# Kernel tuning notes

Hardware: AMD Instinct MI355X
Metric: run time of the kernel (lower is better)

Reference implementation:

```python
import jax, jax.numpy as jnp
import numpy as np

D_MODEL = 1024
N_EXPERTS = 8
HIDDEN = 2048
TOP_K = 2


def setup_inputs() -> dict:
    key = jax.random.key(0)
    ks = jax.random.split(key, 5)
    scale_in = 1.0 / np.sqrt(D_MODEL)
    scale_h = 1.0 / np.sqrt(HIDDEN)
    return {
        "x": jax.random.normal(ks[0], (2, 2048, D_MODEL), dtype=jnp.float32),
        "w_router": jax.random.normal(ks[1], (D_MODEL, N_EXPERTS), dtype=jnp.float32) * scale_in,
        "w1": jax.random.normal(ks[2], (N_EXPERTS, D_MODEL, HIDDEN), dtype=jnp.float32) * scale_in,
        "w3": jax.random.normal(ks[3], (N_EXPERTS, D_MODEL, HIDDEN), dtype=jnp.float32) * scale_in,
        "w2": jax.random.normal(ks[4], (N_EXPERTS, HIDDEN, D_MODEL), dtype=jnp.float32) * scale_h,
    }


def reference(x, w_router, w1, w3, w2):
    orig_shape = x.shape
    xt = x.reshape(-1, orig_shape[-1])            # [T, D]
    T = xt.shape[0]

    # Router: linear -> softmax -> top-k (weights = top-k softmax scores)
    logits = xt @ w_router                         # [T, E]
    scores = jax.nn.softmax(logits, axis=-1)       # [T, E]
    top_w, top_idx = jax.lax.top_k(scores, TOP_K)  # [T, K]

    # Dense routing-weight matrix (reference form of dispatch/combine)
    dense_w = jnp.zeros((T, N_EXPERTS), dtype=scores.dtype)
    dense_w = dense_w.at[jnp.arange(T)[:, None], top_idx].set(top_w)  # [T, E]

    # Per-expert SwiGLU MLP over all tokens (dense reference of grouped GEMM)
    h1 = jnp.einsum('td,edh->teh', xt, w1)         # [T, E, H]
    h3 = jnp.einsum('td,edh->teh', xt, w3)
    h = jax.nn.silu(h1) * h3                       # [T, E, H]
    y = jnp.einsum('teh,ehd->ted', h, w2)          # [T, E, D]

    # Combine with routing weights
    out = jnp.einsum('te,ted->td', dense_w, y)     # [T, D]
    return out.reshape(orig_shape)
```

## Files before the change

### kernel.cpp

```cpp
#include <hip/hip_runtime.h>
#include <stdint.h>

#define D_MODEL 1024
#define N_EXP   8
#define HIDDEN  2048
#define TOPK    2

#define BK    64
#define BM    128
#define BN1   64
#define BN2   128
#define NT1   (D_MODEL / BK)
#define NT2   (HIDDEN / BK)
#define MT_MAX 72
#define G1_GRID (MT_MAX * (HIDDEN / BN1))
#define G2_GRID (MT_MAX * (D_MODEL / BN2))

typedef short bf16x8 __attribute__((ext_vector_type(8)));
typedef float f32x4 __attribute__((ext_vector_type(4)));

__device__ __forceinline__ unsigned short f2bf(float f) {
    union { float f; unsigned u; } v; v.f = f;
    unsigned r = v.u + 0x7fffu + ((v.u >> 16) & 1u);
    return (unsigned short)(r >> 16);
}

__device__ __forceinline__ float bf2f(unsigned short u) {
    union { unsigned u; float f; } v; v.u = (unsigned)u << 16; return v.f;
}

__device__ __forceinline__ void gload_lds16(const void* g, void* l) {
    __builtin_amdgcn_global_load_lds(
        (const __attribute__((address_space(1))) void*)g,
        (__attribute__((address_space(3))) void*)l, 16, 0, 0);
}

__global__ __launch_bounds__(256) void k_router_cvt(
    const float* __restrict__ x, const float* __restrict__ wr,
    unsigned short* __restrict__ xb,
    int* __restrict__ tok_e, float* __restrict__ tok_w,
    int* __restrict__ counts, int T)
{
    int t = blockIdx.x * 4 + (threadIdx.x >> 6);
    int lane = threadIdx.x & 63;
    if (t >= T) return;
    const float4* xr = (const float4*)(x + (size_t)t * D_MODEL);
    float acc[N_EXP];
#pragma unroll
    for (int e = 0; e < N_EXP; ++e) acc[e] = 0.f;
#pragma unroll
    for (int j = 0; j < 4; ++j) {
        int c = j * 64 + lane;
        float4 v = xr[c];
        ushort4 pk;
        pk.x = f2bf(v.x); pk.y = f2bf(v.y); pk.z = f2bf(v.z); pk.w = f2bf(v.w);
        *(ushort4*)(xb + (size_t)t * D_MODEL + c * 4) = pk;
        const float4* w4 = (const float4*)(wr + (size_t)c * 4 * N_EXP);
#pragma unroll
        for (int k = 0; k < 4; ++k) {
            float xv = (k == 0) ? v.x : (k == 1) ? v.y : (k == 2) ? v.z : v.w;
            float4 wa = w4[k * 2], wb = w4[k * 2 + 1];
            acc[0] += xv * wa.x; acc[1] += xv * wa.y; acc[2] += xv * wa.z; acc[3] += xv * wa.w;
            acc[4] += xv * wb.x; acc[5] += xv * wb.y; acc[6] += xv * wb.z; acc[7] += xv * wb.w;
        }
    }
#pragma unroll
    for (int off = 32; off > 0; off >>= 1) {
#pragma unroll
        for (int e = 0; e < N_EXP; ++e) acc[e] += __shfl_down(acc[e], off, 64);
    }
    if (lane == 0) {
        float mx = acc[0];
#pragma unroll
        for (int e = 1; e < N_EXP; ++e) mx = fmaxf(mx, acc[e]);
        float p[N_EXP], den = 0.f;
#pragma unroll
        for (int e = 0; e < N_EXP; ++e) { p[e] = __expf(acc[e] - mx); den += p[e]; }
        float inv = 1.f / den;
        int e0 = 0; float v0 = acc[0];
#pragma unroll
        for (int e = 1; e < N_EXP; ++e) if (acc[e] > v0) { v0 = acc[e]; e0 = e; }
        int e1 = -1; float v1 = -1e30f;
#pragma unroll
        for (int e = 0; e < N_EXP; ++e) if (e != e0 && acc[e] > v1) { v1 = acc[e]; e1 = e; }
        tok_e[2 * t] = e0;     tok_w[2 * t] = p[e0] * inv;
        tok_e[2 * t + 1] = e1; tok_w[2 * t + 1] = p[e1] * inv;
        atomicAdd(&counts[e0], 1);
        atomicAdd(&counts[e1], 1);
    }
}

__global__ __launch_bounds__(256) void k_cvt3(
    const float* __restrict__ w1, const float* __restrict__ w3, const float* __restrict__ w2,
    unsigned short* __restrict__ w1t, unsigned short* __restrict__ w3t, unsigned short* __restrict__ w2t)
{
    __shared__ unsigned short t[64][68];
    const int z = blockIdx.y;
    const int mat = z >> 3, e = z & 7;
    const float* in; unsigned short* out; int Rr, Cc;
    if (mat == 0)      { in = w1; out = w1t; Rr = D_MODEL; Cc = HIDDEN; }
    else if (mat == 1) { in = w3; out = w3t; Rr = D_MODEL; Cc = HIDDEN; }
    else               { in = w2; out = w2t; Rr = HIDDEN; Cc = D_MODEL; }
    const size_t eb = (size_t)e * Rr * Cc;
    const int tpc = Cc >> 6;
    const int bx = blockIdx.x;
    const int c0 = (bx % tpc) * 64, r0 = (bx / tpc) * 64;
    const int tid = threadIdx.x;
#pragma unroll
    for (int p = 0; p < 4; ++p) {
        int li = p * 256 + tid;
        int r = li >> 4, q = li & 15;
        float4 v = *(const float4*)(in + eb + (size_t)(r0 + r) * Cc + c0 + q * 4);
        t[q * 4 + 0][r] = f2bf(v.x);
        t[q * 4 + 1][r] = f2bf(v.y);
        t[q * 4 + 2][r] = f2bf(v.z);
        t[q * 4 + 3][r] = f2bf(v.w);
    }
    __syncthreads();
#pragma unroll
    for (int p = 0; p < 2; ++p) {
        int li = p * 256 + tid;
        int c = li >> 3, j = li & 7;
        bf16x8 v = *(const bf16x8*)(&t[c][j * 8]);
        *(bf16x8*)(&out[eb + (size_t)(c0 + c) * Rr + r0 + j * 8]) = v;
    }
}

__global__ void k_scan_scatter(const int* __restrict__ counts,
                               const int* __restrict__ tok_e, const float* __restrict__ tok_w,
                               int* __restrict__ offs,
                               int* __restrict__ row_token, float* __restrict__ row_weight,
                               int* __restrict__ tok_pos, int T) {
    __shared__ int scurs[N_EXP];
    if (threadIdx.x == 0) {
        int s = 0;
        for (int e = 0; e < N_EXP; ++e) {
            offs[e] = s; scurs[e] = s;
            s += ((counts[e] + BM - 1) / BM) * BM;
        }
        offs[N_EXP] = s;
    }
    __syncthreads();
    for (int i = threadIdx.x; i < 2 * T; i += blockDim.x) {
        int e = tok_e[i];
        int pos = atomicAdd(&scurs[e], 1);
        row_token[pos] = i >> 1;
        row_weight[pos] = tok_w[i];
        tok_pos[i] = pos;
    }
}

__global__ __launch_bounds__(256) void k_gemm1(
    const unsigned short* __restrict__ xb,
    const unsigned short* __restrict__ w1t,
    const unsigned short* __restrict__ w3t,
    const int* __restrict__ row_token,
    const float* __restrict__ row_weight,
    const int* __restrict__ offs,
    unsigned short* __restrict__ h)
{
    __shared__ unsigned short A[BM * BK];
    __shared__ unsigned short B1[BN1 * BK];
    __shared__ unsigned short B3[BN1 * BK];

    const int b = blockIdx.x;
    const int bs = (b & 7) * (G1_GRID / 8) + (b >> 3);
    int e = 0, mt = 0, nt = 0, found = 0, at = 0;
#pragma unroll
    for (int ee = 0; ee < N_EXP; ++ee) {
        int me = (offs[ee + 1] - offs[ee]) >> 7;
        int te = me * (HIDDEN / BN1);
        if (!found && bs < at + te) {
            int loc = bs - at;
            nt = loc / me;
            mt = loc - nt * me;
            e = ee; found = 1;
        }
        at += te;
    }
    if (!found) return;
    const int m0 = offs[e] + mt * BM;
    const int n0 = nt * BN1;

    const int tid = threadIdx.x;
    const int lane = tid & 63, wid = tid >> 6;
    const int wm = wid >> 1, wn = wid & 1;

    const unsigned short* asrc[4];
    unsigned aoff[4];
#pragma unroll
    for (int q = 0; q < 4; ++q) {
        int c = q * 256 + tid;
        int m = c >> 3, kc = c & 7;
        int kcs = kc ^ (m & 7);
        int tok = row_token[m0 + m];
        asrc[q] = xb + (size_t)tok * D_MODEL + kcs * 8;
        aoff[q] = (unsigned)c * 8u;
    }
    const unsigned short* b1src[2];
    const unsigned short* b3src[2];
    unsigned boff[2];
#pragma unroll
    for (int q = 0; q < 2; ++q) {
        int c = q * 256 + tid;
        int n = c >> 3, kc = c & 7;
        int kcs = kc ^ (n & 7);
        b1src[q] = w1t + ((size_t)e * HIDDEN + n0 + n) * D_MODEL + kcs * 8;
        b3src[q] = w3t + ((size_t)e * HIDDEN + n0 + n) * D_MODEL + kcs * 8;
        boff[q] = (unsigned)c * 8u;
    }

    f32x4 acc1[4][2], acc3[4][2];
    const f32x4 zf = {0.f, 0.f, 0.f, 0.f};
#pragma unroll
    for (int mi = 0; mi < 4; ++mi)
#pragma unroll
        for (int ni = 0; ni < 2; ++ni) { acc1[mi][ni] = zf; acc3[mi][ni] = zf; }

    for (int kt = 0; kt < NT1; ++kt) {
        const int ko = kt * BK;
#pragma unroll
        for (int q = 0; q < 4; ++q) gload_lds16(asrc[q] + ko, &A[aoff[q]]);
#pragma unroll
        for (int q = 0; q < 2; ++q) {
            gload_lds16(b1src[q] + ko, &B1[boff[q]]);
            gload_lds16(b3src[q] + ko, &B3[boff[q]]);
        }
        __syncthreads();
#pragma unroll
        for (int kf = 0; kf < 2; ++kf) {
            bf16x8 a[4], b1f[2], b3f[2];
            int ke = kf * 32 + (lane >> 4) * 8;
#pragma unroll
            for (int mi = 0; mi < 4; ++mi) {
                int m = wm * 64 + mi * 16 + (lane & 15);
                a[mi] = *(const bf16x8*)(&A[m * BK + (ke ^ ((m & 7) * 8))]);
            }
#pragma unroll
            for (int ni = 0; ni < 2; ++ni) {
                int n = wn * 32 + ni * 16 + (lane & 15);
                int eo = n * BK + (ke ^ ((n & 7) * 8));
                b1f[ni] = *(const bf16x8*)(&B1[eo]);
                b3f[ni] = *(const bf16x8*)(&B3[eo]);
            }
#pragma unroll
            for (int mi = 0; mi < 4; ++mi)
#pragma unroll
                for (int ni = 0; ni < 2; ++ni) {
                    acc1[mi][ni] = __builtin_amdgcn_mfma_f32_16x16x32_bf16(a[mi], b1f[ni], acc1[mi][ni], 0, 0, 0);
                    acc3[mi][ni] = __builtin_amdgcn_mfma_f32_16x16x32_bf16(a[mi], b3f[ni], acc3[mi][ni], 0, 0, 0);
                }
        }
        __syncthreads();
    }

#pragma unroll
    for (int mi = 0; mi < 4; ++mi) {
#pragma unroll
        for (int r = 0; r < 4; ++r) {
            int m = wm * 64 + mi * 16 + (lane >> 4) * 4 + r;
            float wgt = row_weight[m0 + m];
            size_t rowbase = (size_t)(m0 + m) * HIDDEN + n0;
#pragma unroll
            for (int ni = 0; ni < 2; ++ni) {
                float v1 = acc1[mi][ni][r], v3 = acc3[mi][ni][r];
                float sv = v1 / (1.f + __expf(-v1));
                int n = wn * 32 + ni * 16 + (lane & 15);
                h[rowbase + n] = f2bf(sv * v3 * wgt);
            }
        }
    }
}

__global__ __launch_bounds__(256) void k_gemm2(
    const unsigned short* __restrict__ h,
    const unsigned short* __restrict__ w2t,
    const int* __restrict__ offs,
    unsigned short* __restrict__ y)
{
    __shared__ unsigned short A[BM * BK];
    __shared__ unsigned short B[BN2 * BK];

    const int b = blockIdx.x;
    const int bs = (b & 7) * (G2_GRID / 8) + (b >> 3);
    int e = 0, mt = 0, nt = 0, found = 0, at = 0;
#pragma unroll
    for (int ee = 0; ee < N_EXP; ++ee) {
        int me = (offs[ee + 1] - offs[ee]) >> 7;
        int te = me * (D_MODEL / BN2);
        if (!found && bs < at + te) {
            int loc = bs - at;
            nt = loc / me;
            mt = loc - nt * me;
            e = ee; found = 1;
        }
        at += te;
    }
    if (!found) return;
    const int m0 = offs[e] + mt * BM;
    const int n0 = nt * BN2;

    const int tid = threadIdx.x;
    const int lane = tid & 63, wid = tid >> 6;
    const int wm = wid >> 1, wn = wid & 1;

    const unsigned short* asrc[4];
    unsigned aoff[4];
#pragma unroll
    for (int q = 0; q < 4; ++q) {
        int c = q * 256 + tid;
        int m = c >> 3, kc = c & 7;
        int kcs = kc ^ (m & 7);
        asrc[q] = h + (size_t)(m0 + m) * HIDDEN + kcs * 8;
        aoff[q] = (unsigned)c * 8u;
    }
    const unsigned short* bsrc[4];
    unsigned boff[4];
#pragma unroll
    for (int q = 0; q < 4; ++q) {
        int c = q * 256 + tid;
        int n = c >> 3, kc = c & 7;
        int kcs = kc ^ (n & 7);
        bsrc[q] = w2t + ((size_t)e * D_MODEL + n0 + n) * HIDDEN + kcs * 8;
        boff[q] = (unsigned)c * 8u;
    }

    f32x4 acc[4][4];
    const f32x4 zf = {0.f, 0.f, 0.f, 0.f};
#pragma unroll
    for (int mi = 0; mi < 4; ++mi)
#pragma unroll
        for (int ni = 0; ni < 4; ++ni) acc[mi][ni] = zf;

    for (int kt = 0; kt < NT2; ++kt) {
        const int ko = kt * BK;
#pragma unroll
        for (int q = 0; q < 4; ++q) gload_lds16(asrc[q] + ko, &A[aoff[q]]);
#pragma unroll
        for (int q = 0; q < 4; ++q) gload_lds16(bsrc[q] + ko, &B[boff[q]]);
        __syncthreads();
#pragma unroll
        for (int kf = 0; kf < 2; ++kf) {
            bf16x8 a[4], bfr[4];
            int ke = kf * 32 + (lane >> 4) * 8;
#pragma unroll
            for (int mi = 0; mi < 4; ++mi) {
                int m = wm * 64 + mi * 16 + (lane & 15);
                a[mi] = *(const bf16x8*)(&A[m * BK + (ke ^ ((m & 7) * 8))]);
            }
#pragma unroll
            for (int ni = 0; ni < 4; ++ni) {
                int n = wn * 64 + ni * 16 + (lane & 15);
                bfr[ni] = *(const bf16x8*)(&B[n * BK + (ke ^ ((n & 7) * 8))]);
            }
#pragma unroll
            for (int mi = 0; mi < 4; ++mi)
#pragma unroll
                for (int ni = 0; ni < 4; ++ni)
                    acc[mi][ni] = __builtin_amdgcn_mfma_f32_16x16x32_bf16(a[mi], bfr[ni], acc[mi][ni], 0, 0, 0);
        }
        __syncthreads();
    }

#pragma unroll
    for (int mi = 0; mi < 4; ++mi) {
#pragma unroll
        for (int r = 0; r < 4; ++r) {
            int m = wm * 64 + mi * 16 + (lane >> 4) * 4 + r;
            size_t rowbase = (size_t)(m0 + m) * D_MODEL + n0;
#pragma unroll
            for (int ni = 0; ni < 4; ++ni) {
                int n = wn * 64 + ni * 16 + (lane & 15);
                y[rowbase + n] = f2bf(acc[mi][ni][r]);
            }
        }
    }
}

__global__ void k_combine(const unsigned short* __restrict__ y,
                          const int* __restrict__ tok_pos,
                          float* __restrict__ out, int n8) {
    int i = blockIdx.x * blockDim.x + threadIdx.x;
    if (i >= n8) return;
    int t = i >> 7;
    int c = (i & 127) * 8;
    int p0 = tok_pos[2 * t];
    int p1 = tok_pos[2 * t + 1];
    bf16x8 v0 = *(const bf16x8*)(y + (size_t)p0 * D_MODEL + c);
    bf16x8 v1 = *(const bf16x8*)(y + (size_t)p1 * D_MODEL + c);
    float* op = out + (size_t)t * D_MODEL + c;
    float4 o0, o1;
    o0.x = bf2f((unsigned short)v0[0]) + bf2f((unsigned short)v1[0]);
    o0.y = bf2f((unsigned short)v0[1]) + bf2f((unsigned short)v1[1]);
    o0.z = bf2f((unsigned short)v0[2]) + bf2f((unsigned short)v1[2]);
    o0.w = bf2f((unsigned short)v0[3]) + bf2f((unsigned short)v1[3]);
    o1.x = bf2f((unsigned short)v0[4]) + bf2f((unsigned short)v1[4]);
    o1.y = bf2f((unsigned short)v0[5]) + bf2f((unsigned short)v1[5]);
    o1.z = bf2f((unsigned short)v0[6]) + bf2f((unsigned short)v1[6]);
    o1.w = bf2f((unsigned short)v0[7]) + bf2f((unsigned short)v1[7]);
    *(float4*)op = o0;
    *(float4*)(op + 4) = o1;
}

extern "C" void kernel_launch(void* const* d_in, const int* in_sizes, int n_in,
                              void* d_out, int out_size, void* d_ws, size_t ws_size,
                              hipStream_t stream) {
    const float* x  = (const float*)d_in[0];
    const float* wr = (const float*)d_in[1];
    const float* w1 = (const float*)d_in[2];
    const float* w3 = (const float*)d_in[3];
    const float* w2 = (const float*)d_in[4];
    float* out = (float*)d_out;

    const int T = in_sizes[0] / D_MODEL;
    const int Rp = T * TOPK + N_EXP * BM;

    char* ws = (char*)d_ws;
    size_t o = 0;
    unsigned short* xb  = (unsigned short*)(ws + o); o += (size_t)T * D_MODEL * 2;
    unsigned short* h   = (unsigned short*)(ws + o); o += (size_t)Rp * HIDDEN * 2;
    unsigned short* w1t = (unsigned short*)(ws + o); o += (size_t)N_EXP * D_MODEL * HIDDEN * 2;
    unsigned short* w3t = (unsigned short*)(ws + o); o += (size_t)N_EXP * D_MODEL * HIDDEN * 2;
    unsigned short* w2t = (unsigned short*)(ws + o); o += (size_t)N_EXP * HIDDEN * D_MODEL * 2;
    int*   row_token  = (int*)(ws + o);   o += (size_t)Rp * 4;
    float* row_weight = (float*)(ws + o); o += (size_t)Rp * 4;
    int*   tok_e      = (int*)(ws + o);   o += (size_t)2 * T * 4;
    float* tok_w      = (float*)(ws + o); o += (size_t)2 * T * 4;
    int*   tok_pos    = (int*)(ws + o);   o += (size_t)2 * T * 4;
    int*   counts     = (int*)(ws + o);   o += 16 * 4;
    int*   offs       = (int*)(ws + o);   o += 16 * 4;

    unsigned short* y = w1t;

    hipMemsetAsync(counts, 0, 16 * 4, stream);
    hipMemsetAsync(row_token, 0, (size_t)Rp * 4, stream);
    hipMemsetAsync(row_weight, 0, (size_t)Rp * 4, stream);

    k_router_cvt<<<(T + 3) / 4, 256, 0, stream>>>(x, wr, xb, tok_e, tok_w, counts, T);

    dim3 gc(512, 24);
    k_cvt3<<<gc, 256, 0, stream>>>(w1, w3, w2, w1t, w3t, w2t);

    k_scan_scatter<<<1, 1024, 0, stream>>>(counts, tok_e, tok_w, offs,
                                           row_token, row_weight, tok_pos, T);

    k_gemm1<<<G1_GRID, 256, 0, stream>>>(xb, w1t, w3t, row_token, row_weight, offs, h);
    k_gemm2<<<G2_GRID, 256, 0, stream>>>(h, w2t, offs, y);

    int n8 = T * D_MODEL / 8;
    k_combine<<<(n8 + 255) / 256, 256, 0, stream>>>(y, tok_pos, out, n8);
}
```

Measured before the change: 339.4 us.

## Interleave w1/w3 weights, enlarge GEMM tiles to 256 and double-buffer LDS

The weight-conversion kernel now writes w1 and w3 interleaved in 16-row groups into one combined matrix, so gemm1 loads a single B tile that covers both gate and up projections. Both GEMMs move to 512-thread blocks with larger tiles (256x256 in gemm1, 128x256 in gemm2), double-buffered LDS prefetch and s_setprio around the MFMA loops. Expert padding grows to 256 rows. The aim is more data reuse per tile and overlap of global-to-LDS loads with compute, at the cost of more padded rows, higher register and LDS pressure, and fewer blocks.

```diff
diff --git a/kernel.cpp b/kernel.cpp
--- a/kernel.cpp
+++ b/kernel.cpp
@@ -7,14 +7,14 @@
 #define TOPK    2
 
 #define BK    64
-#define BM    128
-#define BN1   64
-#define BN2   128
+#define PADM  256
 #define NT1   (D_MODEL / BK)
 #define NT2   (HIDDEN / BK)
-#define MT_MAX 72
-#define G1_GRID (MT_MAX * (HIDDEN / BN1))
-#define G2_GRID (MT_MAX * (D_MODEL / BN2))
+#define MT1_MAX 40
+#define NB1   (2 * HIDDEN / 256)
+#define G1_GRID (MT1_MAX * NB1)
+#define MT2_MAX 80
+#define G2_GRID (MT2_MAX * (D_MODEL / 256))
 
 typedef short bf16x8 __attribute__((ext_vector_type(8)));
 typedef float f32x4 __attribute__((ext_vector_type(4)));
@@ -92,16 +92,16 @@
 
 __global__ __launch_bounds__(256) void k_cvt3(
     const float* __restrict__ w1, const float* __restrict__ w3, const float* __restrict__ w2,
-    unsigned short* __restrict__ w1t, unsigned short* __restrict__ w3t, unsigned short* __restrict__ w2t)
+    unsigned short* __restrict__ w13t, unsigned short* __restrict__ w2t)
 {
     __shared__ unsigned short t[64][68];
     const int z = blockIdx.y;
     const int mat = z >> 3, e = z & 7;
-    const float* in; unsigned short* out; int Rr, Cc;
-    if (mat == 0)      { in = w1; out = w1t; Rr = D_MODEL; Cc = HIDDEN; }
-    else if (mat == 1) { in = w3; out = w3t; Rr = D_MODEL; Cc = HIDDEN; }
-    else               { in = w2; out = w2t; Rr = HIDDEN; Cc = D_MODEL; }
-    const size_t eb = (size_t)e * Rr * Cc;
+    const float* in; int Rr, Cc;
+    if (mat == 0)      { in = w1; Rr = D_MODEL; Cc = HIDDEN; }
+    else if (mat == 1) { in = w3; Rr = D_MODEL; Cc = HIDDEN; }
+    else               { in = w2; Rr = HIDDEN; Cc = D_MODEL; }
+    const size_t eb_in = (size_t)e * Rr * Cc;
     const int tpc = Cc >> 6;
     const int bx = blockIdx.x;
     const int c0 = (bx % tpc) * 64, r0 = (bx / tpc) * 64;
@@ -110,19 +110,34 @@
     for (int p = 0; p < 4; ++p) {
         int li = p * 256 + tid;
         int r = li >> 4, q = li & 15;
-        float4 v = *(const float4*)(in + eb + (size_t)(r0 + r) * Cc + c0 + q * 4);
+        float4 v = *(const float4*)(in + eb_in + (size_t)(r0 + r) * Cc + c0 + q * 4);
         t[q * 4 + 0][r] = f2bf(v.x);
         t[q * 4 + 1][r] = f2bf(v.y);
         t[q * 4 + 2][r] = f2bf(v.z);
         t[q * 4 + 3][r] = f2bf(v.w);
     }
     __syncthreads();
-#pragma unroll
-    for (int p = 0; p < 2; ++p) {
-        int li = p * 256 + tid;
-        int c = li >> 3, j = li & 7;
-        bf16x8 v = *(const bf16x8*)(&t[c][j * 8]);
-        *(bf16x8*)(&out[eb + (size_t)(c0 + c) * Rr + r0 + j * 8]) = v;
+    if (mat < 2) {
+        const size_t eb = (size_t)e * (2 * HIDDEN) * D_MODEL;
+        const int moff = mat ? 16 : 0;
+#pragma unroll
+        for (int p = 0; p < 2; ++p) {
+            int li = p * 256 + tid;
+            int c = li >> 3, j = li & 7;
+            int C = c0 + c;
+            int r13 = ((C >> 4) << 5) + moff + (C & 15);
+            bf16x8 v = *(const bf16x8*)(&t[c][j * 8]);
+            *(bf16x8*)(&w13t[eb + (size_t)r13 * D_MODEL + r0 + j * 8]) = v;
+        }
+    } else {
+        const size_t eb = (size_t)e * D_MODEL * HIDDEN;
+#pragma unroll
+        for (int p = 0; p < 2; ++p) {
+            int li = p * 256 + tid;
+            int c = li >> 3, j = li & 7;
+            bf16x8 v = *(const bf16x8*)(&t[c][j * 8]);
+            *(bf16x8*)(&w2t[eb + (size_t)(c0 + c) * HIDDEN + r0 + j * 8]) = v;
+        }
     }
 }
 
@@ -136,7 +151,7 @@
         int s = 0;
         for (int e = 0; e < N_EXP; ++e) {
             offs[e] = s; scurs[e] = s;
-            s += ((counts[e] + BM - 1) / BM) * BM;
+            s += ((counts[e] + PADM - 1) / PADM) * PADM;
         }
         offs[N_EXP] = s;
     }
@@ -150,26 +165,24 @@
     }
 }
 
-__global__ __launch_bounds__(256) void k_gemm1(
+__global__ __launch_bounds__(512, 2) void k_gemm1(
     const unsigned short* __restrict__ xb,
-    const unsigned short* __restrict__ w1t,
-    const unsigned short* __restrict__ w3t,
+    const unsigned short* __restrict__ w13t,
     const int* __restrict__ row_token,
     const float* __restrict__ row_weight,
     const int* __restrict__ offs,
     unsigned short* __restrict__ h)
 {
-    __shared__ unsigned short A[BM * BK];
-    __shared__ unsigned short B1[BN1 * BK];
-    __shared__ unsigned short B3[BN1 * BK];
+    __shared__ unsigned short A[2][256 * BK];
+    __shared__ unsigned short B[2][256 * BK];
 
     const int b = blockIdx.x;
     const int bs = (b & 7) * (G1_GRID / 8) + (b >> 3);
     int e = 0, mt = 0, nt = 0, found = 0, at = 0;
 #pragma unroll
     for (int ee = 0; ee < N_EXP; ++ee) {
-        int me = (offs[ee + 1] - offs[ee]) >> 7;
-        int te = me * (HIDDEN / BN1);
+        int me = (offs[ee + 1] - offs[ee]) >> 8;
+        int te = me * NB1;
         if (!found && bs < at + te) {
             int loc = bs - at;
             nt = loc / me;
@@ -179,107 +192,111 @@
         at += te;
     }
     if (!found) return;
-    const int m0 = offs[e] + mt * BM;
-    const int n0 = nt * BN1;
+    const int m0 = offs[e] + mt * 256;
+    const int n0b = nt * 256;
 
     const int tid = threadIdx.x;
     const int lane = tid & 63, wid = tid >> 6;
-    const int wm = wid >> 1, wn = wid & 1;
+    const int wm = wid >> 2, wn = wid & 3;
 
     const unsigned short* asrc[4];
     unsigned aoff[4];
 #pragma unroll
     for (int q = 0; q < 4; ++q) {
-        int c = q * 256 + tid;
+        int c = q * 512 + tid;
         int m = c >> 3, kc = c & 7;
         int kcs = kc ^ (m & 7);
         int tok = row_token[m0 + m];
         asrc[q] = xb + (size_t)tok * D_MODEL + kcs * 8;
         aoff[q] = (unsigned)c * 8u;
     }
-    const unsigned short* b1src[2];
-    const unsigned short* b3src[2];
-    unsigned boff[2];
-#pragma unroll
-    for (int q = 0; q < 2; ++q) {
-        int c = q * 256 + tid;
+    const unsigned short* bsrc[4];
+    unsigned boff[4];
+#pragma unroll
+    for (int q = 0; q < 4; ++q) {
+        int c = q * 512 + tid;
         int n = c >> 3, kc = c & 7;
         int kcs = kc ^ (n & 7);
-        b1src[q] = w1t + ((size_t)e * HIDDEN + n0 + n) * D_MODEL + kcs * 8;
-        b3src[q] = w3t + ((size_t)e * HIDDEN + n0 + n) * D_MODEL + kcs * 8;
+        bsrc[q] = w13t + ((size_t)e * (2 * HIDDEN) + n0b + n) * D_MODEL + kcs * 8;
         boff[q] = (unsigned)c * 8u;
     }
 
-    f32x4 acc1[4][2], acc3[4][2];
+    f32x4 acc[8][4];
     const f32x4 zf = {0.f, 0.f, 0.f, 0.f};
 #pragma unroll
-    for (int mi = 0; mi < 4; ++mi)
-#pragma unroll
-        for (int ni = 0; ni < 2; ++ni) { acc1[mi][ni] = zf; acc3[mi][ni] = zf; }
+    for (int mi = 0; mi < 8; ++mi)
+#pragma unroll
+        for (int ni = 0; ni < 4; ++ni) acc[mi][ni] = zf;
+
+#pragma unroll
+    for (int q = 0; q < 4; ++q) {
+        gload_lds16(asrc[q], &A[0][aoff[q]]);
+        gload_lds16(bsrc[q], &B[0][boff[q]]);
+    }
+    __syncthreads();
 
     for (int kt = 0; kt < NT1; ++kt) {
-        const int ko = kt * BK;
-#pragma unroll
-        for (int q = 0; q < 4; ++q) gload_lds16(asrc[q] + ko, &A[aoff[q]]);
-#pragma unroll
-        for (int q = 0; q < 2; ++q) {
-            gload_lds16(b1src[q] + ko, &B1[boff[q]]);
-            gload_lds16(b3src[q] + ko, &B3[boff[q]]);
+        const int cur = kt & 1;
+        if (kt + 1 < NT1) {
+            const int ko = (kt + 1) * BK;
+#pragma unroll
+            for (int q = 0; q < 4; ++q) {
+                gload_lds16(asrc[q] + ko, &A[cur ^ 1][aoff[q]]);
+                gload_lds16(bsrc[q] + ko, &B[cur ^ 1][boff[q]]);
+            }
+        }
+#pragma unroll
+        for (int kf = 0; kf < 2; ++kf) {
+            bf16x8 a[8], bf[4];
+            int ke = kf * 32 + (lane >> 4) * 8;
+#pragma unroll
+            for (int mi = 0; mi < 8; ++mi) {
+                int m = wm * 128 + mi * 16 + (lane & 15);
+                a[mi] = *(const bf16x8*)(&A[cur][m * BK + (ke ^ ((m & 7) * 8))]);
+            }
+#pragma unroll
+            for (int ni = 0; ni < 4; ++ni) {
+                int n = wn * 64 + ni * 16 + (lane & 15);
+                bf[ni] = *(const bf16x8*)(&B[cur][n * BK + (ke ^ ((n & 7) * 8))]);
+            }
+            __builtin_amdgcn_s_setprio(1);
+#pragma unroll
+            for (int mi = 0; mi < 8; ++mi)
+#pragma unroll
+                for (int ni = 0; ni < 4; ++ni)
+                    acc[mi][ni] = __builtin_amdgcn_mfma_f32_16x16x32_bf16(a[mi], bf[ni], acc[mi][ni], 0, 0, 0);
+            __builtin_amdgcn_s_setprio(0);
         }
         __syncthreads();
-#pragma unroll
-        for (int kf = 0; kf < 2; ++kf) {
-            bf16x8 a[4], b1f[2], b3f[2];
-            int ke = kf * 32 + (lane >> 4) * 8;
-#pragma unroll
-            for (int mi = 0; mi < 4; ++mi) {
-                int m = wm * 64 + mi * 16 + (lane & 15);
-                a[mi] = *(const bf16x8*)(&A[m * BK + (ke ^ ((m & 7) * 8))]);
-            }
-#pragma unroll
-            for (int ni = 0; ni < 2; ++ni) {
-                int n = wn * 32 + ni * 16 + (lane & 15);
-                int eo = n * BK + (ke ^ ((n & 7) * 8));
-                b1f[ni] = *(const bf16x8*)(&B1[eo]);
-                b3f[ni] = *(const bf16x8*)(&B3[eo]);
-            }
-#pragma unroll
-            for (int mi = 0; mi < 4; ++mi)
-#pragma unroll
-                for (int ni = 0; ni < 2; ++ni) {
-                    acc1[mi][ni] = __builtin_amdgcn_mfma_f32_16x16x32_bf16(a[mi], b1f[ni], acc1[mi][ni], 0, 0, 0);
-                    acc3[mi][ni] = __builtin_amdgcn_mfma_f32_16x16x32_bf16(a[mi], b3f[ni], acc3[mi][ni], 0, 0, 0);
-                }
-        }
-        __syncthreads();
-    }
-
-#pragma unroll
-    for (int mi = 0; mi < 4; ++mi) {
+    }
+
+    const int g0 = (n0b + wn * 64) >> 5;
+#pragma unroll
+    for (int mi = 0; mi < 8; ++mi) {
 #pragma unroll
         for (int r = 0; r < 4; ++r) {
-            int m = wm * 64 + mi * 16 + (lane >> 4) * 4 + r;
+            int m = wm * 128 + mi * 16 + (lane >> 4) * 4 + r;
             float wgt = row_weight[m0 + m];
-            size_t rowbase = (size_t)(m0 + m) * HIDDEN + n0;
-#pragma unroll
-            for (int ni = 0; ni < 2; ++ni) {
-                float v1 = acc1[mi][ni][r], v3 = acc3[mi][ni][r];
+            size_t rowbase = (size_t)(m0 + m) * HIDDEN;
+#pragma unroll
+            for (int p = 0; p < 2; ++p) {
+                float v1 = acc[mi][2 * p][r], v3 = acc[mi][2 * p + 1][r];
                 float sv = v1 / (1.f + __expf(-v1));
-                int n = wn * 32 + ni * 16 + (lane & 15);
-                h[rowbase + n] = f2bf(sv * v3 * wgt);
-            }
-        }
-    }
-}
-
-__global__ __launch_bounds__(256) void k_gemm2(
+                int hc = (g0 + p) * 16 + (lane & 15);
+                h[rowbase + hc] = f2bf(sv * v3 * wgt);
+            }
+        }
+    }
+}
+
+__global__ __launch_bounds__(512, 2) void k_gemm2(
     const unsigned short* __restrict__ h,
     const unsigned short* __restrict__ w2t,
     const int* __restrict__ offs,
     unsigned short* __restrict__ y)
 {
-    __shared__ unsigned short A[BM * BK];
-    __shared__ unsigned short B[BN2 * BK];
+    __shared__ unsigned short A[2][128 * BK];
+    __shared__ unsigned short B[2][256 * BK];
 
     const int b = blockIdx.x;
     const int bs = (b & 7) * (G2_GRID / 8) + (b >> 3);
@@ -287,7 +304,7 @@
 #pragma unroll
     for (int ee = 0; ee < N_EXP; ++ee) {
         int me = (offs[ee + 1] - offs[ee]) >> 7;
-        int te = me * (D_MODEL / BN2);
+        int te = me * (D_MODEL / 256);
         if (!found && bs < at + te) {
             int loc = bs - at;
             nt = loc / me;
@@ -297,18 +314,18 @@
         at += te;
     }
     if (!found) return;
-    const int m0 = offs[e] + mt * BM;
-    const int n0 = nt * BN2;
+    const int m0 = offs[e] + mt * 128;
+    const int n0 = nt * 256;
 
     const int tid = threadIdx.x;
     const int lane = tid & 63, wid = tid >> 6;
-    const int wm = wid >> 1, wn = wid & 1;
-
-    const unsigned short* asrc[4];
-    unsigned aoff[4];
-#pragma unroll
-    for (int q = 0; q < 4; ++q) {
-        int c = q * 256 + tid;
+    const int wm = wid >> 2, wn = wid & 3;
+
+    const unsigned short* asrc[2];
+    unsigned aoff[2];
+#pragma unroll
+    for (int q = 0; q < 2; ++q) {
+        int c = q * 512 + tid;
         int m = c >> 3, kc = c & 7;
         int kcs = kc ^ (m & 7);
         asrc[q] = h + (size_t)(m0 + m) * HIDDEN + kcs * 8;
@@ -318,7 +335,7 @@
     unsigned boff[4];
 #pragma unroll
     for (int q = 0; q < 4; ++q) {
-        int c = q * 256 + tid;
+        int c = q * 512 + tid;
         int n = c >> 3, kc = c & 7;
         int kcs = kc ^ (n & 7);
         bsrc[q] = w2t + ((size_t)e * D_MODEL + n0 + n) * HIDDEN + kcs * 8;
@@ -332,32 +349,42 @@
 #pragma unroll
         for (int ni = 0; ni < 4; ++ni) acc[mi][ni] = zf;
 
+#pragma unroll
+    for (int q = 0; q < 2; ++q) gload_lds16(asrc[q], &A[0][aoff[q]]);
+#pragma unroll
+    for (int q = 0; q < 4; ++q) gload_lds16(bsrc[q], &B[0][boff[q]]);
+    __syncthreads();
+
     for (int kt = 0; kt < NT2; ++kt) {
-        const int ko = kt * BK;
-#pragma unroll
-        for (int q = 0; q < 4; ++q) gload_lds16(asrc[q] + ko, &A[aoff[q]]);
-#pragma unroll
-        for (int q = 0; q < 4; ++q) gload_lds16(bsrc[q] + ko, &B[boff[q]]);
-        __syncthreads();
+        const int cur = kt & 1;
+        if (kt + 1 < NT2) {
+            const int ko = (kt + 1) * BK;
+#pragma unroll
+            for (int q = 0; q < 2; ++q) gload_lds16(asrc[q] + ko, &A[cur ^ 1][aoff[q]]);
+#pragma unroll
+            for (int q = 0; q < 4; ++q) gload_lds16(bsrc[q] + ko, &B[cur ^ 1][boff[q]]);
+        }
 #pragma unroll
         for (int kf = 0; kf < 2; ++kf) {
-            bf16x8 a[4], bfr[4];
+            bf16x8 a[4], bf[4];
             int ke = kf * 32 + (lane >> 4) * 8;
 #pragma unroll
             for (int mi = 0; mi < 4; ++mi) {
                 int m = wm * 64 + mi * 16 + (lane & 15);
-                a[mi] = *(const bf16x8*)(&A[m * BK + (ke ^ ((m & 7) * 8))]);
+                a[mi] = *(const bf16x8*)(&A[cur][m * BK + (ke ^ ((m & 7) * 8))]);
             }
 #pragma unroll
             for (int ni = 0; ni < 4; ++ni) {
                 int n = wn * 64 + ni * 16 + (lane & 15);
-                bfr[ni] = *(const bf16x8*)(&B[n * BK + (ke ^ ((n & 7) * 8))]);
-            }
+                bf[ni] = *(const bf16x8*)(&B[cur][n * BK + (ke ^ ((n & 7) * 8))]);
+            }
+            __builtin_amdgcn_s_setprio(1);
 #pragma unroll
             for (int mi = 0; mi < 4; ++mi)
 #pragma unroll
                 for (int ni = 0; ni < 4; ++ni)
-                    acc[mi][ni] = __builtin_amdgcn_mfma_f32_16x16x32_bf16(a[mi], bfr[ni], acc[mi][ni], 0, 0, 0);
+                    acc[mi][ni] = __builtin_amdgcn_mfma_f32_16x16x32_bf16(a[mi], bf[ni], acc[mi][ni], 0, 0, 0);
+            __builtin_amdgcn_s_setprio(0);
         }
         __syncthreads();
     }
@@ -413,15 +440,14 @@
     float* out = (float*)d_out;
 
     const int T = in_sizes[0] / D_MODEL;
-    const int Rp = T * TOPK + N_EXP * BM;
+    const int Rp = T * TOPK + N_EXP * PADM;
 
     char* ws = (char*)d_ws;
     size_t o = 0;
-    unsigned short* xb  = (unsigned short*)(ws + o); o += (size_t)T * D_MODEL * 2;
-    unsigned short* h   = (unsigned short*)(ws + o); o += (size_t)Rp * HIDDEN * 2;
-    unsigned short* w1t = (unsigned short*)(ws + o); o += (size_t)N_EXP * D_MODEL * HIDDEN * 2;
-    unsigned short* w3t = (unsigned short*)(ws + o); o += (size_t)N_EXP * D_MODEL * HIDDEN * 2;
-    unsigned short* w2t = (unsigned short*)(ws + o); o += (size_t)N_EXP * HIDDEN * D_MODEL * 2;
+    unsigned short* xb   = (unsigned short*)(ws + o); o += (size_t)T * D_MODEL * 2;
+    unsigned short* h    = (unsigned short*)(ws + o); o += (size_t)Rp * HIDDEN * 2;
+    unsigned short* w13t = (unsigned short*)(ws + o); o += (size_t)N_EXP * 2 * HIDDEN * D_MODEL * 2;
+    unsigned short* w2t  = (unsigned short*)(ws + o); o += (size_t)N_EXP * D_MODEL * HIDDEN * 2;
     int*   row_token  = (int*)(ws + o);   o += (size_t)Rp * 4;
     float* row_weight = (float*)(ws + o); o += (size_t)Rp * 4;
     int*   tok_e      = (int*)(ws + o);   o += (size_t)2 * T * 4;
@@ -430,7 +456,7 @@
     int*   counts     = (int*)(ws + o);   o += 16 * 4;
     int*   offs       = (int*)(ws + o);   o += 16 * 4;
 
-    unsigned short* y = w1t;
+    unsigned short* y = w13t;
 
     hipMemsetAsync(counts, 0, 16 * 4, stream);
     hipMemsetAsync(row_token, 0, (size_t)Rp * 4, stream);
@@ -439,13 +465,13 @@
     k_router_cvt<<<(T + 3) / 4, 256, 0, stream>>>(x, wr, xb, tok_e, tok_w, counts, T);
 
     dim3 gc(512, 24);
-    k_cvt3<<<gc, 256, 0, stream>>>(w1, w3, w2, w1t, w3t, w2t);
+    k_cvt3<<<gc, 256, 0, stream>>>(w1, w3, w2, w13t, w2t);
 
     k_scan_scatter<<<1, 1024, 0, stream>>>(counts, tok_e, tok_w, offs,
                                            row_token, row_weight, tok_pos, T);
 
-    k_gemm1<<<G1_GRID, 256, 0, stream>>>(xb, w1t, w3t, row_token, row_weight, offs, h);
-    k_gemm2<<<G2_GRID, 256, 0, stream>>>(h, w2t, offs, y);
+    k_gemm1<<<G1_GRID, 512, 0, stream>>>(xb, w13t, row_token, row_weight, offs, h);
+    k_gemm2<<<G2_GRID, 512, 0, stream>>>(h, w2t, offs, y);
 
     int n8 = T * D_MODEL / 8;
     k_combine<<<(n8 + 255) / 256, 256, 0, stream>>>(y, tok_pos, out, n8);
```

Result: slower. 383.6 us (+13.0%).

## Fuse fp32 weight conversion into grouped GEMMs with double-buffered larger tiles

Applied to the files above, without the earlier changes.

Drops the separate weight transpose/convert kernel. Both GEMMs now read the fp32 expert weights directly, convert them in registers with packed bf16 conversion, and store them transposed and swizzled into LDS. The GEMMs move to 512-thread blocks with larger N tiles (128 for gemm1, 256 for gemm2), double-buffered LDS, register prefetch of the next K tile, and setprio around the MFMAs. This removes a full weight read and write pass, but each tile re-reads fp32 weights (twice the bytes of bf16) once per M tile. It also adds per-tile conversion work inside the main loop.

```diff
diff --git a/kernel.cpp b/kernel.cpp
--- a/kernel.cpp
+++ b/kernel.cpp
@@ -7,14 +7,11 @@
 #define TOPK    2
 
 #define BK    64
-#define BM    128
-#define BN1   64
-#define BN2   128
+#define PADM  128
 #define NT1   (D_MODEL / BK)
 #define NT2   (HIDDEN / BK)
-#define MT_MAX 72
-#define G1_GRID (MT_MAX * (HIDDEN / BN1))
-#define G2_GRID (MT_MAX * (D_MODEL / BN2))
+#define G1X   1152
+#define G2X   288
 
 typedef short bf16x8 __attribute__((ext_vector_type(8)));
 typedef float f32x4 __attribute__((ext_vector_type(4)));
@@ -29,13 +26,19 @@
     union { unsigned u; float f; } v; v.u = (unsigned)u << 16; return v.f;
 }
 
+__device__ __forceinline__ unsigned cvtpk(float a, float b) {
+    unsigned r;
+    asm("v_cvt_pk_bf16_f32 %0, %1, %2" : "=v"(r) : "v"(a), "v"(b));
+    return r;
+}
+
 __device__ __forceinline__ void gload_lds16(const void* g, void* l) {
     __builtin_amdgcn_global_load_lds(
         (const __attribute__((address_space(1))) void*)g,
         (__attribute__((address_space(3))) void*)l, 16, 0, 0);
 }
 
-__global__ __launch_bounds__(256) void k_router_cvt(
+__global__ __launch_bounds__(256) void k_pre(
     const float* __restrict__ x, const float* __restrict__ wr,
     unsigned short* __restrict__ xb,
     int* __restrict__ tok_e, float* __restrict__ tok_w,
@@ -90,42 +93,6 @@
     }
 }
 
-__global__ __launch_bounds__(256) void k_cvt3(
-    const float* __restrict__ w1, const float* __restrict__ w3, const float* __restrict__ w2,
-    unsigned short* __restrict__ w1t, unsigned short* __restrict__ w3t, unsigned short* __restrict__ w2t)
-{
-    __shared__ unsigned short t[64][68];
-    const int z = blockIdx.y;
-    const int mat = z >> 3, e = z & 7;
-    const float* in; unsigned short* out; int Rr, Cc;
-    if (mat == 0)      { in = w1; out = w1t; Rr = D_MODEL; Cc = HIDDEN; }
-    else if (mat == 1) { in = w3; out = w3t; Rr = D_MODEL; Cc = HIDDEN; }
-    else               { in = w2; out = w2t; Rr = HIDDEN; Cc = D_MODEL; }
-    const size_t eb = (size_t)e * Rr * Cc;
-    const int tpc = Cc >> 6;
-    const int bx = blockIdx.x;
-    const int c0 = (bx % tpc) * 64, r0 = (bx / tpc) * 64;
-    const int tid = threadIdx.x;
-#pragma unroll
-    for (int p = 0; p < 4; ++p) {
-        int li = p * 256 + tid;
-        int r = li >> 4, q = li & 15;
-        float4 v = *(const float4*)(in + eb + (size_t)(r0 + r) * Cc + c0 + q * 4);
-        t[q * 4 + 0][r] = f2bf(v.x);
-        t[q * 4 + 1][r] = f2bf(v.y);
-        t[q * 4 + 2][r] = f2bf(v.z);
-        t[q * 4 + 3][r] = f2bf(v.w);
-    }
-    __syncthreads();
-#pragma unroll
-    for (int p = 0; p < 2; ++p) {
-        int li = p * 256 + tid;
-        int c = li >> 3, j = li & 7;
-        bf16x8 v = *(const bf16x8*)(&t[c][j * 8]);
-        *(bf16x8*)(&out[eb + (size_t)(c0 + c) * Rr + r0 + j * 8]) = v;
-    }
-}
-
 __global__ void k_scan_scatter(const int* __restrict__ counts,
                                const int* __restrict__ tok_e, const float* __restrict__ tok_w,
                                int* __restrict__ offs,
@@ -136,7 +103,7 @@
         int s = 0;
         for (int e = 0; e < N_EXP; ++e) {
             offs[e] = s; scurs[e] = s;
-            s += ((counts[e] + BM - 1) / BM) * BM;
+            s += ((counts[e] + PADM - 1) / PADM) * PADM;
         }
         offs[N_EXP] = s;
     }
@@ -150,26 +117,26 @@
     }
 }
 
-__global__ __launch_bounds__(256) void k_gemm1(
+__global__ __launch_bounds__(512, 1) void k_gemm1(
     const unsigned short* __restrict__ xb,
-    const unsigned short* __restrict__ w1t,
-    const unsigned short* __restrict__ w3t,
+    const float* __restrict__ w1,
+    const float* __restrict__ w3,
     const int* __restrict__ row_token,
     const float* __restrict__ row_weight,
     const int* __restrict__ offs,
     unsigned short* __restrict__ h)
 {
-    __shared__ unsigned short A[BM * BK];
-    __shared__ unsigned short B1[BN1 * BK];
-    __shared__ unsigned short B3[BN1 * BK];
+    __shared__ unsigned short A[2][128 * BK];
+    __shared__ unsigned short B1[2][128 * BK];
+    __shared__ unsigned short B3[2][128 * BK];
 
     const int b = blockIdx.x;
-    const int bs = (b & 7) * (G1_GRID / 8) + (b >> 3);
+    const int bs = (b & 7) * (G1X / 8) + (b >> 3);
     int e = 0, mt = 0, nt = 0, found = 0, at = 0;
 #pragma unroll
     for (int ee = 0; ee < N_EXP; ++ee) {
         int me = (offs[ee + 1] - offs[ee]) >> 7;
-        int te = me * (HIDDEN / BN1);
+        int te = me * 16;
         if (!found && bs < at + te) {
             int loc = bs - at;
             nt = loc / me;
@@ -179,36 +146,31 @@
         at += te;
     }
     if (!found) return;
-    const int m0 = offs[e] + mt * BM;
-    const int n0 = nt * BN1;
+    const int m0 = offs[e] + mt * 128;
+    const int n0 = nt * 128;
 
     const int tid = threadIdx.x;
     const int lane = tid & 63, wid = tid >> 6;
-    const int wm = wid >> 1, wn = wid & 1;
-
-    const unsigned short* asrc[4];
-    unsigned aoff[4];
-#pragma unroll
-    for (int q = 0; q < 4; ++q) {
-        int c = q * 256 + tid;
+    const int wm = wid >> 2, wn = wid & 3;
+
+    const unsigned short* asrc[2];
+    unsigned aoff[2];
+#pragma unroll
+    for (int q = 0; q < 2; ++q) {
+        int c = q * 512 + tid;
         int m = c >> 3, kc = c & 7;
         int kcs = kc ^ (m & 7);
         int tok = row_token[m0 + m];
         asrc[q] = xb + (size_t)tok * D_MODEL + kcs * 8;
         aoff[q] = (unsigned)c * 8u;
     }
-    const unsigned short* b1src[2];
-    const unsigned short* b3src[2];
-    unsigned boff[2];
-#pragma unroll
-    for (int q = 0; q < 2; ++q) {
-        int c = q * 256 + tid;
-        int n = c >> 3, kc = c & 7;
-        int kcs = kc ^ (n & 7);
-        b1src[q] = w1t + ((size_t)e * HIDDEN + n0 + n) * D_MODEL + kcs * 8;
-        b3src[q] = w3t + ((size_t)e * HIDDEN + n0 + n) * D_MODEL + kcs * 8;
-        boff[q] = (unsigned)c * 8u;
-    }
+
+    const int kpb = tid >> 5;
+    const int n4b = tid & 31;
+    const float* w1e = w1 + (size_t)e * D_MODEL * HIDDEN + n0 + n4b * 4;
+    const float* w3e = w3 + (size_t)e * D_MODEL * HIDDEN + n0 + n4b * 4;
+
+    f32x4 r1lo[2], r1hi[2], r3lo[2], r3hi[2];
 
     f32x4 acc1[4][2], acc3[4][2];
     const f32x4 zf = {0.f, 0.f, 0.f, 0.f};
@@ -217,16 +179,56 @@
 #pragma unroll
         for (int ni = 0; ni < 2; ++ni) { acc1[mi][ni] = zf; acc3[mi][ni] = zf; }
 
+#pragma unroll
+    for (int p = 0; p < 2; ++p) {
+        size_t rb = (size_t)(2 * (p * 16 + kpb)) * HIDDEN;
+        r1lo[p] = *(const f32x4*)(w1e + rb);
+        r1hi[p] = *(const f32x4*)(w1e + rb + HIDDEN);
+        r3lo[p] = *(const f32x4*)(w3e + rb);
+        r3hi[p] = *(const f32x4*)(w3e + rb + HIDDEN);
+    }
+    gload_lds16(asrc[0], &A[0][aoff[0]]);
+    gload_lds16(asrc[1], &A[0][aoff[1]]);
+
+    int cur = 0;
+#pragma unroll 1
     for (int kt = 0; kt < NT1; ++kt) {
-        const int ko = kt * BK;
-#pragma unroll
-        for (int q = 0; q < 4; ++q) gload_lds16(asrc[q] + ko, &A[aoff[q]]);
-#pragma unroll
-        for (int q = 0; q < 2; ++q) {
-            gload_lds16(b1src[q] + ko, &B1[boff[q]]);
-            gload_lds16(b3src[q] + ko, &B3[boff[q]]);
-        }
-        __syncthreads();
+        asm volatile("s_waitcnt vmcnt(0)" ::: "memory");
+        unsigned* B1u = (unsigned*)&B1[cur][0];
+        unsigned* B3u = (unsigned*)&B3[cur][0];
+#pragma unroll
+        for (int p = 0; p < 2; ++p) {
+            int kp = p * 16 + kpb;
+#pragma unroll
+            for (int j = 0; j < 4; ++j) {
+                int n = n4b * 4 + j;
+                unsigned col = (unsigned)kp ^ ((((unsigned)n >> 1) & 7u) << 2);
+                B1u[n * 32 + col] = cvtpk(r1lo[p][j], r1hi[p][j]);
+                B3u[n * 32 + col] = cvtpk(r3lo[p][j], r3hi[p][j]);
+            }
+        }
+        asm volatile("s_waitcnt lgkmcnt(0)" ::: "memory");
+        __builtin_amdgcn_s_barrier();
+
+        if (kt + 1 < NT1) {
+            const size_t kgo = (size_t)((kt + 1) * BK) * HIDDEN;
+#pragma unroll
+            for (int p = 0; p < 2; ++p) {
+                size_t rb = kgo + (size_t)(2 * (p * 16 + kpb)) * HIDDEN;
+                r1lo[p] = *(const f32x4*)(w1e + rb);
+                r1hi[p] = *(const f32x4*)(w1e + rb + HIDDEN);
+                r3lo[p] = *(const f32x4*)(w3e + rb);
+                r3hi[p] = *(const f32x4*)(w3e + rb + HIDDEN);
+            }
+            const int ko = (kt + 1) * BK;
+            gload_lds16(asrc[0] + ko, &A[cur ^ 1][aoff[0]]);
+            gload_lds16(asrc[1] + ko, &A[cur ^ 1][aoff[1]]);
+        }
+        __builtin_amdgcn_sched_barrier(0);
+
+        const unsigned short* Ac = &A[cur][0];
+        const unsigned short* B1c = &B1[cur][0];
+        const unsigned short* B3c = &B3[cur][0];
 #pragma unroll
         for (int kf = 0; kf < 2; ++kf) {
             bf16x8 a[4], b1f[2], b3f[2];
@@ -234,15 +236,16 @@
 #pragma unroll
             for (int mi = 0; mi < 4; ++mi) {
                 int m = wm * 64 + mi * 16 + (lane & 15);
-                a[mi] = *(const bf16x8*)(&A[m * BK + (ke ^ ((m & 7) * 8))]);
+                a[mi] = *(const bf16x8*)(&Ac[m * BK + (ke ^ ((m & 7) * 8))]);
             }
 #pragma unroll
             for (int ni = 0; ni < 2; ++ni) {
                 int n = wn * 32 + ni * 16 + (lane & 15);
-                int eo = n * BK + (ke ^ ((n & 7) * 8));
-                b1f[ni] = *(const bf16x8*)(&B1[eo]);
-                b3f[ni] = *(const bf16x8*)(&B3[eo]);
-            }
+                int eo = n * BK + (ke ^ ((((unsigned)n >> 1) & 7u) << 3));
+                b1f[ni] = *(const bf16x8*)(&B1c[eo]);
+                b3f[ni] = *(const bf16x8*)(&B3c[eo]);
+            }
+            __builtin_amdgcn_s_setprio(1);
 #pragma unroll
             for (int mi = 0; mi < 4; ++mi)
 #pragma unroll
@@ -250,8 +253,9 @@
                     acc1[mi][ni] = __builtin_amdgcn_mfma_f32_16x16x32_bf16(a[mi], b1f[ni], acc1[mi][ni], 0, 0, 0);
                     acc3[mi][ni] = __builtin_amdgcn_mfma_f32_16x16x32_bf16(a[mi], b3f[ni], acc3[mi][ni], 0, 0, 0);
                 }
-        }
-        __syncthreads();
+            __builtin_amdgcn_s_setprio(0);
+        }
+        cur ^= 1;
     }
 
 #pragma unroll
@@ -272,22 +276,22 @@
     }
 }
 
-__global__ __launch_bounds__(256) void k_gemm2(
-    const unsigned short* __restrict__ h,
-    const unsigned short* __restrict__ w2t,
+__global__ __launch_bounds__(512, 1) void k_gemm2(
+    const unsigned short* __restrict__ hh,
+    const float* __restrict__ w2,
     const int* __restrict__ offs,
     unsigned short* __restrict__ y)
 {
-    __shared__ unsigned short A[BM * BK];
-    __shared__ unsigned short B[BN2 * BK];
+    __shared__ unsigned short A[2][128 * BK];
+    __shared__ unsigned short B[2][256 * BK];
 
     const int b = blockIdx.x;
-    const int bs = (b & 7) * (G2_GRID / 8) + (b >> 3);
+    const int bs = (b & 7) * (G2X / 8) + (b >> 3);
     int e = 0, mt = 0, nt = 0, found = 0, at = 0;
 #pragma unroll
     for (int ee = 0; ee < N_EXP; ++ee) {
         int me = (offs[ee + 1] - offs[ee]) >> 7;
-        int te = me * (D_MODEL / BN2);
+        int te = me * 4;
         if (!found && bs < at + te) {
             int loc = bs - at;
             nt = loc / me;
@@ -297,33 +301,27 @@
         at += te;
     }
     if (!found) return;
-    const int m0 = offs[e] + mt * BM;
-    const int n0 = nt * BN2;
+    const int m0 = offs[e] + mt * 128;
+    const int n0 = nt * 256;
 
     const int tid = threadIdx.x;
     const int lane = tid & 63, wid = tid >> 6;
-    const int wm = wid >> 1, wn = wid & 1;
-
-    const unsigned short* asrc[4];
-    unsigned aoff[4];
-#pragma unroll
-    for (int q = 0; q < 4; ++q) {
-        int c = q * 256 + tid;
+    const int wm = wid >> 2, wn = wid & 3;
+
+    const unsigned short* asrc[2];
+    unsigned aoff[2];
+#pragma unroll
+    for (int q = 0; q < 2; ++q) {
+        int c = q * 512 + tid;
         int m = c >> 3, kc = c & 7;
         int kcs = kc ^ (m & 7);
-        asrc[q] = h + (size_t)(m0 + m) * HIDDEN + kcs * 8;
+        asrc[q] = hh + (size_t)(m0 + m) * HIDDEN + kcs * 8;
         aoff[q] = (unsigned)c * 8u;
     }
-    const unsigned short* bsrc[4];
-    unsigned boff[4];
-#pragma unroll
-    for (int q = 0; q < 4; ++q) {
-        int c = q * 256 + tid;
-        int n = c >> 3, kc = c & 7;
-        int kcs = kc ^ (n & 7);
-        bsrc[q] = w2t + ((size_t)e * D_MODEL + n0 + n) * HIDDEN + kcs * 8;
-        boff[q] = (unsigned)c * 8u;
-    }
+
+    const float* w2e = w2 + (size_t)e * HIDDEN * D_MODEL + n0 + lane * 4;
+
+    f32x4 rlo[4], rhi[4];
 
     f32x4 acc[4][4];
     const f32x4 zf = {0.f, 0.f, 0.f, 0.f};
@@ -332,34 +330,73 @@
 #pragma unroll
         for (int ni = 0; ni < 4; ++ni) acc[mi][ni] = zf;
 
+#pragma unroll
+    for (int p = 0; p < 4; ++p) {
+        size_t rb = (size_t)(2 * (p * 8 + wid)) * D_MODEL;
+        rlo[p] = *(const f32x4*)(w2e + rb);
+        rhi[p] = *(const f32x4*)(w2e + rb + D_MODEL);
+    }
+    gload_lds16(asrc[0], &A[0][aoff[0]]);
+    gload_lds16(asrc[1], &A[0][aoff[1]]);
+
+    int cur = 0;
+#pragma unroll 1
     for (int kt = 0; kt < NT2; ++kt) {
-        const int ko = kt * BK;
-#pragma unroll
-        for (int q = 0; q < 4; ++q) gload_lds16(asrc[q] + ko, &A[aoff[q]]);
-#pragma unroll
-        for (int q = 0; q < 4; ++q) gload_lds16(bsrc[q] + ko, &B[boff[q]]);
-        __syncthreads();
+        asm volatile("s_waitcnt vmcnt(0)" ::: "memory");
+        unsigned* Bu = (unsigned*)&B[cur][0];
+#pragma unroll
+        for (int p = 0; p < 4; ++p) {
+            int kp = p * 8 + wid;
+#pragma unroll
+            for (int j = 0; j < 4; ++j) {
+                int n = lane * 4 + j;
+                unsigned col = (unsigned)kp ^ ((((unsigned)n >> 1) & 7u) << 2);
+                Bu[n * 32 + col] = cvtpk(rlo[p][j], rhi[p][j]);
+            }
+        }
+        asm volatile("s_waitcnt lgkmcnt(0)" ::: "memory");
+        __builtin_amdgcn_s_barrier();
+
+        if (kt + 1 < NT2) {
+            const size_t kgo = (size_t)((kt + 1) * BK) * D_MODEL;
+#pragma unroll
+            for (int p = 0; p < 4; ++p) {
+                size_t rb = kgo + (size_t)(2 * (p * 8 + wid)) * D_MODEL;
+                rlo[p] = *(const f32x4*)(w2e + rb);
+                rhi[p] = *(const f32x4*)(w2e + rb + D_MODEL);
+            }
+            const int ko = (kt + 1) * BK;
+            gload_lds16(asrc[0] + ko, &A[cur ^ 1][aoff[0]]);
+            gload_lds16(asrc[1] + ko, &A[cur ^ 1][aoff[1]]);
+        }
+        __builtin_amdgcn_sched_barrier(0);
+
+        const unsigned short* Ac = &A[cur][0];
+        const unsigned short* Bc = &B[cur][0];
 #pragma unroll
         for (int kf = 0; kf < 2; ++kf) {
-            bf16x8 a[4], bfr[4];
+            bf16x8 a[4], bf[4];
             int ke = kf * 32 + (lane >> 4) * 8;
 #pragma unroll
             for (int mi = 0; mi < 4; ++mi) {
                 int m = wm * 64 + mi * 16 + (lane & 15);
-                a[mi] = *(const bf16x8*)(&A[m * BK + (ke ^ ((m & 7) * 8))]);
+                a[mi] = *(const bf16x8*)(&Ac[m * BK + (ke ^ ((m & 7) * 8))]);
             }
 #pragma unroll
             for (int ni = 0; ni < 4; ++ni) {
                 int n = wn * 64 + ni * 16 + (lane & 15);
-                bfr[ni] = *(const bf16x8*)(&B[n * BK + (ke ^ ((n & 7) * 8))]);
-            }
+                int eo = n * BK + (ke ^ ((((unsigned)n >> 1) & 7u) << 3));
+                bf[ni] = *(const bf16x8*)(&Bc[eo]);
+            }
+            __builtin_amdgcn_s_setprio(1);
 #pragma unroll
             for (int mi = 0; mi < 4; ++mi)
 #pragma unroll
                 for (int ni = 0; ni < 4; ++ni)
-                    acc[mi][ni] = __builtin_amdgcn_mfma_f32_16x16x32_bf16(a[mi], bfr[ni], acc[mi][ni], 0, 0, 0);
-        }
-        __syncthreads();
+                    acc[mi][ni] = __builtin_amdgcn_mfma_f32_16x16x32_bf16(a[mi], bf[ni], acc[mi][ni], 0, 0, 0);
+            __builtin_amdgcn_s_setprio(0);
+        }
+        cur ^= 1;
     }
 
 #pragma unroll
@@ -413,15 +450,13 @@
     float* out = (float*)d_out;
 
     const int T = in_sizes[0] / D_MODEL;
-    const int Rp = T * TOPK + N_EXP * BM;
+    const int Rp = T * TOPK + N_EXP * PADM;
 
     char* ws = (char*)d_ws;
     size_t o = 0;
-    unsigned short* xb  = (unsigned short*)(ws + o); o += (size_t)T * D_MODEL * 2;
-    unsigned short* h   = (unsigned short*)(ws + o); o += (size_t)Rp * HIDDEN * 2;
-    unsigned short* w1t = (unsigned short*)(ws + o); o += (size_t)N_EXP * D_MODEL * HIDDEN * 2;
-    unsigned short* w3t = (unsigned short*)(ws + o); o += (size_t)N_EXP * D_MODEL * HIDDEN * 2;
-    unsigned short* w2t = (unsigned short*)(ws + o); o += (size_t)N_EXP * HIDDEN * D_MODEL * 2;
+    unsigned short* xb = (unsigned short*)(ws + o); o += (size_t)T * D_MODEL * 2;
+    unsigned short* h  = (unsigned short*)(ws + o); o += (size_t)Rp * HIDDEN * 2;
+    unsigned short* y  = (unsigned short*)(ws + o); o += (size_t)Rp * D_MODEL * 2;
     int*   row_token  = (int*)(ws + o);   o += (size_t)Rp * 4;
     float* row_weight = (float*)(ws + o); o += (size_t)Rp * 4;
     int*   tok_e      = (int*)(ws + o);   o += (size_t)2 * T * 4;
@@ -430,22 +465,17 @@
     int*   counts     = (int*)(ws + o);   o += 16 * 4;
     int*   offs       = (int*)(ws + o);   o += 16 * 4;
 
-    unsigned short* y = w1t;
-
     hipMemsetAsync(counts, 0, 16 * 4, stream);
     hipMemsetAsync(row_token, 0, (size_t)Rp * 4, stream);
     hipMemsetAsync(row_weight, 0, (size_t)Rp * 4, stream);
 
-    k_router_cvt<<<(T + 3) / 4, 256, 0, stream>>>(x, wr, xb, tok_e, tok_w, counts, T);
-
-    dim3 gc(512, 24);
-    k_cvt3<<<gc, 256, 0, stream>>>(w1, w3, w2, w1t, w3t, w2t);
+    k_pre<<<(T + 3) / 4, 256, 0, stream>>>(x, wr, xb, tok_e, tok_w, counts, T);
 
     k_scan_scatter<<<1, 1024, 0, stream>>>(counts, tok_e, tok_w, offs,
                                            row_token, row_weight, tok_pos, T);
 
-    k_gemm1<<<G1_GRID, 256, 0, stream>>>(xb, w1t, w3t, row_token, row_weight, offs, h);
-    k_gemm2<<<G2_GRID, 256, 0, stream>>>(h, w2t, offs, y);
+    k_gemm1<<<G1X, 512, 0, stream>>>(xb, w1, w3, row_token, row_weight, offs, h);
+    k_gemm2<<<G2X, 512, 0, stream>>>(h, w2, offs, y);
 
     int n8 = T * D_MODEL / 8;
     k_combine<<<(n8 + 255) / 256, 256, 0, stream>>>(y, tok_pos, out, n8);
```

After: 519.8 us. 53.2% more time.
